# Optimization experiments

Measured on AMD Instinct MI355X. Metric: run time of the kernel, lower is better.

Reference implementation:

```python
import jax, jax.numpy as jnp
import numpy as np

B, TED, G, N, E, MD, NOISE = 10000, 512, 64, 2000, 64000, 15, 128
PAC = 10
PACDIM = (TED + NOISE) * PAC  # 6400
D0, D1 = 1024, 512


def _linear_params(k, fan_in, fan_out):
    kw, kb = jax.random.split(k)
    lim = 1.0 / np.sqrt(fan_in)
    w = jax.random.uniform(kw, (fan_in, fan_out), minval=-lim, maxval=lim, dtype=jnp.float32)
    b = jax.random.uniform(kb, (fan_out,), minval=-lim, maxval=lim, dtype=jnp.float32)
    return w, b


def setup_inputs() -> dict:
    key = jax.random.key(0)
    ks = jax.random.split(key, 12)
    inp = {
        'input_': jax.random.normal(ks[0], (B, TED), dtype=jnp.float32),
        'graphs_x': jax.random.normal(ks[1], (G, N, 1), dtype=jnp.float32),
        'edge_index': jax.random.randint(ks[2], (G, 2, E), 0, N, dtype=jnp.int32),
        'graph_ids': jax.random.randint(ks[3], (B,), 0, G, dtype=jnp.int32),
        'chain': jax.random.normal(ks[4], (B, 1), dtype=jnp.float32),
        'metadata': jax.random.normal(ks[5], (B, MD), dtype=jnp.float32),
    }
    inp['gcn_w'], inp['gcn_b'] = _linear_params(ks[6], 1, 1)
    inp['meta_w'], inp['meta_b'] = _linear_params(ks[7], 1 + MD, 32)
    inp['gme_w'], inp['gme_b'] = _linear_params(ks[8], N + 32, NOISE)
    inp['seq_w0'], inp['seq_b0'] = _linear_params(ks[9], PACDIM, D0)
    inp['seq_w1'], inp['seq_b1'] = _linear_params(ks[10], D0, D1)
    inp['seq_w2'], inp['seq_b2'] = _linear_params(ks[11], D1, 1)
    return inp


def _gcn_one(x, ei, gcn_w, gcn_b):
    # GCNConv(1,1) with self-loops and symmetric normalization.
    loops = jnp.arange(N, dtype=ei.dtype)
    src = jnp.concatenate([ei[0], loops])
    dst = jnp.concatenate([ei[1], loops])
    deg = jax.ops.segment_sum(jnp.ones_like(src, dtype=x.dtype), dst, num_segments=N)
    dinv = jax.lax.rsqrt(deg)  # deg >= 1 due to self-loops
    norm = dinv[src] * dinv[dst]  # [E+N]
    xw = x @ gcn_w  # [N,1]
    msg = xw[src] * norm[:, None]
    out = jax.ops.segment_sum(msg, dst, num_segments=N) + gcn_b
    return out.reshape(-1)  # flatten -> [N]


def reference(input_, graphs_x, edge_index, graph_ids, chain, metadata,
              gcn_w, gcn_b, meta_w, meta_b, gme_w, gme_b,
              seq_w0, seq_b0, seq_w1, seq_b1, seq_w2, seq_b2):
    # per-unique-graph GCN, vectorized over G graphs
    gcn_out = jax.vmap(lambda x, ei: _gcn_one(x, ei, gcn_w, gcn_b))(graphs_x, edge_index)  # [G,N]
    graph_emb = gcn_out[graph_ids]  # gather: [B,N]
    all_meta = jnp.concatenate([chain, metadata], axis=1)  # [B,1+MD]
    meta_emb = jax.nn.relu(all_meta @ meta_w + meta_b)  # [B,32]
    noise = jnp.concatenate([graph_emb, meta_emb], axis=1) @ gme_w + gme_b  # [B,NOISE]
    h = jnp.concatenate([input_, noise], axis=1).reshape(-1, PACDIM)  # [B/PAC, PACDIM]
    h = jax.nn.leaky_relu(h @ seq_w0 + seq_b0, 0.2)  # dropout omitted (eval mode)
    h = jax.nn.leaky_relu(h @ seq_w1 + seq_b1, 0.2)
    return h @ seq_w2 + seq_b2  # [B/PAC, 1]
```

## Files before the change

### kernel.cpp

```cpp
#include <hip/hip_runtime.h>

typedef __bf16 bf16_t;
typedef __bf16 bf16x4 __attribute__((ext_vector_type(4)));
typedef __bf16 bf16x8 __attribute__((ext_vector_type(8)));
typedef float floatx4 __attribute__((ext_vector_type(4)));

#define G_GRAPHS 64
#define N_NODES 2000
#define N_EDGES 64000
#define BATCH 10000
#define TED_ 512
#define NOISE_ 128
#define PACDIM_ 6400
#define D0_ 1024
#define D1_ 512
#define MROWS 1000
#define ESPLIT 8
#define EPB (N_EDGES / ESPLIT)
#define MSPLIT 8
#define S0 8

#define DEG_BLKS 512
#define PACK_BLKS 625
#define MSG_BLKS 512
#define W0T_BLKS 1600
#define W1T_BLKS 128

__device__ __forceinline__ void glds16(const void* g, void* l) {
    __builtin_amdgcn_global_load_lds(
        (__attribute__((address_space(1))) void*)(g),
        (__attribute__((address_space(3))) void*)(l), 16, 0, 0);
}

__global__ __launch_bounds__(512) void deg_pack_kernel(
    const int* __restrict__ edge_index, float* __restrict__ degs_part,
    const float* __restrict__ in, bf16_t* __restrict__ A)
{
    __shared__ float h[N_NODES];
    const int b = blockIdx.x, tid = threadIdx.x;
    if (b < DEG_BLKS) {
        const int s = b & 7, g = b >> 3;
        for (int n = tid; n < N_NODES; n += 512) h[n] = 0.f;
        __syncthreads();
        const int4* d4 = (const int4*)(edge_index + (size_t)g * 2 * N_EDGES
                                       + N_EDGES + s * EPB);
        for (int e = tid; e < EPB / 4; e += 512) {
            int4 v = d4[e];
            atomicAdd(&h[v.x], 1.0f); atomicAdd(&h[v.y], 1.0f);
            atomicAdd(&h[v.z], 1.0f); atomicAdd(&h[v.w], 1.0f);
        }
        __syncthreads();
        float* dp = degs_part + ((size_t)g * ESPLIT + s) * N_NODES;
        for (int n = tid; n < N_NODES; n += 512) dp[n] = h[n];
        return;
    }
    {
        int base = (b - DEG_BLKS) * 2048;
        for (int u = 0; u < 4; u++) {
            int idx = base + u * 512 + tid;
            float4 v = ((const float4*)in)[idx];
            int bb = idx >> 7;
            int c = (idx & 127) << 2;
            int r = bb / 10, slot = bb - r * 10;
            bf16x4 o = { (bf16_t)v.x, (bf16_t)v.y, (bf16_t)v.z, (bf16_t)v.w };
            *(bf16x4*)(A + (size_t)r * PACDIM_ + slot * 640 + c) = o;
        }
    }
}

__global__ __launch_bounds__(512) void work_kernel(
    const float* __restrict__ graphs_x, const int* __restrict__ edge_index,
    const float* __restrict__ degs_part, float* __restrict__ outs_part,
    const float* __restrict__ W0, bf16_t* __restrict__ W0t,
    const float* __restrict__ W1, bf16_t* __restrict__ W1t)
{
    __shared__ __align__(16) float sm[3 * N_NODES];
    const int b = blockIdx.x, tid = threadIdx.x;

    if (b < MSG_BLKS) {
        float* ys  = sm;
        float* dvl = sm + N_NODES;
        float* oh  = sm + 2 * N_NODES;
        const int s = b & 7, g = b >> 3;
        const float* xg = graphs_x + (size_t)g * N_NODES;
        const float* dgp = degs_part + (size_t)g * ESPLIT * N_NODES;
        for (int n = tid; n < N_NODES; n += 512) {
            float d = 1.0f;
            for (int p = 0; p < ESPLIT; p++) d += dgp[(size_t)p * N_NODES + n];
            float dv = rsqrtf(d);
            dvl[n] = dv;
            ys[n] = xg[n] * dv;
            oh[n] = 0.f;
        }
        __syncthreads();
        const int* src = edge_index + (size_t)g * 2 * N_EDGES + s * EPB;
        const int2* s2 = (const int2*)src;
        const int2* d2 = (const int2*)(src + N_EDGES);
        for (int e = tid; e < EPB / 2; e += 512) {
            int2 sv = s2[e], dd = d2[e];
            atomicAdd(&oh[dd.x], ys[sv.x] * dvl[dd.x]);
            atomicAdd(&oh[dd.y], ys[sv.y] * dvl[dd.y]);
        }
        __syncthreads();
        float* op = outs_part + ((size_t)g * MSPLIT + s) * N_NODES;
        for (int n = tid; n < N_NODES; n += 512) op[n] = oh[n];
        return;
    }
    float (*t)[67] = (float(*)[67])sm;
    const float* W; bf16_t* Wt; int Rr, Cc, r0, c0;
    if (b < MSG_BLKS + W0T_BLKS) {
        int tile = b - MSG_BLKS;
        W = W0; Wt = W0t; Rr = PACDIM_; Cc = D0_;
        r0 = (tile >> 4) << 6; c0 = (tile & 15) << 6;
    } else {
        int tile = b - (MSG_BLKS + W0T_BLKS);
        W = W1; Wt = W1t; Rr = D0_; Cc = D1_;
        r0 = (tile >> 3) << 6; c0 = (tile & 7) << 6;
    }
    for (int u = 0; u < 2; u++) {
        int idx = u * 512 + tid;
        int r = idx >> 4, c4 = (idx & 15) << 2;
        float4 v = *(const float4*)(W + (size_t)(r0 + r) * Cc + c0 + c4);
        t[r][c4] = v.x; t[r][c4 + 1] = v.y; t[r][c4 + 2] = v.z; t[r][c4 + 3] = v.w;
    }
    __syncthreads();
    {
        int c = tid >> 3, seg = tid & 7;
        bf16x8 o;
        for (int jj = 0; jj < 8; jj++) o[jj] = (bf16_t)t[seg * 8 + jj][c];
        *(bf16x8*)(Wt + (size_t)(c0 + c) * Rr + r0 + seg * 8) = o;
    }
}

__global__ __launch_bounds__(512) void gnoise_kernel(
    const float* __restrict__ graphs_x, const float* __restrict__ degs_part,
    const float* __restrict__ outs_part,
    const float* __restrict__ gcn_w, const float* __restrict__ gcn_b,
    const float* __restrict__ gme_w, float* __restrict__ gnoise_p)
{
    __shared__ float of[500];
    __shared__ float part[4][128];
    const int s = blockIdx.x, g = blockIdx.y, tid = threadIdx.x;
    const int nBase = s * 500;
    const float w = gcn_w[0], bb = gcn_b[0];
    const float* dgp = degs_part + (size_t)g * ESPLIT * N_NODES;
    const float* otp = outs_part + (size_t)g * MSPLIT * N_NODES;
    for (int n = tid; n < 500; n += 512) {
        int gn = nBase + n;
        float d = 1.0f, o = 0.f;
        for (int p = 0; p < ESPLIT; p++) d += dgp[(size_t)p * N_NODES + gn];
        for (int p = 0; p < MSPLIT; p++) o += otp[(size_t)p * N_NODES + gn];
        of[n] = w * (o + graphs_x[(size_t)g * N_NODES + gn] / d) + bb;
    }
    __syncthreads();
    const int j = tid & 127, ch = tid >> 7;
    float acc = 0.f;
    const int n0 = ch * 125;
    for (int n = n0; n < n0 + 125; n++)
        acc += of[n] * gme_w[(size_t)(nBase + n) * 128 + j];
    part[ch][j] = acc;
    __syncthreads();
    if (tid < 128)
        gnoise_p[((size_t)g * 4 + s) * 128 + tid] =
            part[0][tid] + part[1][tid] + part[2][tid] + part[3][tid];
}

__global__ __launch_bounds__(256) void meta_kernel(
    const float* __restrict__ chain, const float* __restrict__ metadata,
    const int* __restrict__ graph_ids,
    const float* __restrict__ meta_w, const float* __restrict__ meta_b,
    const float* __restrict__ gme_w, const float* __restrict__ gme_b,
    const float* __restrict__ gnoise_p, bf16_t* __restrict__ A)
{
    int wid = (blockIdx.x * 256 + threadIdx.x) >> 6;
    int lane = threadIdx.x & 63;
    if (wid >= BATCH) return;
    const int b = wid;
    float me = 0.f;
    if (lane < 32) {
        me = meta_b[lane] + chain[b] * meta_w[lane];
        for (int i = 1; i < 16; i++)
            me += metadata[(size_t)b * 15 + (i - 1)] * meta_w[(size_t)i * 32 + lane];
        me = me > 0.f ? me : 0.f;
    }
    const int gid = graph_ids[b];
    const float* gp = gnoise_p + (size_t)gid * 4 * 128;
    const int j1 = lane, j2 = lane + 64;
    float n1 = gme_b[j1] + gp[j1] + gp[128 + j1] + gp[256 + j1] + gp[384 + j1];
    float n2 = gme_b[j2] + gp[j2] + gp[128 + j2] + gp[256 + j2] + gp[384 + j2];
    for (int k = 0; k < 32; k++) {
        float mk = __shfl(me, k, 64);
        const float* wrow = gme_w + (size_t)(N_NODES + k) * 128;
        n1 += mk * wrow[j1];
        n2 += mk * wrow[j2];
    }
    int r = b / 10, slot = b - r * 10;
    bf16_t* dp = A + (size_t)r * PACDIM_ + slot * 640 + TED_;
    dp[j1] = (bf16_t)n1;
    dp[j2] = (bf16_t)n2;
}

__global__ __launch_bounds__(256) void gemm_bt_splitk_kernel(
    const bf16_t* __restrict__ A,
    const bf16_t* __restrict__ Bt,
    float* __restrict__ P,
    int M, int N, int K, int KS, int zbits, int xbits, int Mp)
{
    __shared__ __align__(16) bf16_t As[2][128 * 32];
    __shared__ __align__(16) bf16_t Bs[2][128 * 32];
    const int tid = threadIdx.x;
    const int wave = tid >> 6;
    const int lane = tid & 63;
    const int id = blockIdx.x;
    const int z = id & ((1 << zbits) - 1);
    const int xt = (id >> zbits) & ((1 << xbits) - 1);
    const int yt = id >> (zbits + xbits);
    const int mBase = yt * 128;
    const int nBase = xt * 128;
    const int wm = (wave & 1) * 64;
    const int wn = (wave >> 1) * 64;

    floatx4 acc[4][4] = {};

    const int rA0 = tid >> 2;
    const int g4 = tid & 3;
    const int f4 = (rA0 >> 1) & 3;
    const int k8 = (g4 ^ f4) * 8;
    int gm0 = mBase + rA0;      if (gm0 > M - 1) gm0 = M - 1;
    int gm1 = mBase + 64 + rA0; if (gm1 > M - 1) gm1 = M - 1;
    const bf16_t* aP0 = A + (size_t)gm0 * K + k8;
    const bf16_t* aP1 = A + (size_t)gm1 * K + k8;
    const bf16_t* bP0 = Bt + (size_t)(nBase + rA0) * K + k8;
    const bf16_t* bP1 = Bt + (size_t)(nBase + 64 + rA0) * K + k8;

    const int q4 = lane >> 4;
    const int mr = lane & 15;
    const int kq = ((q4 ^ ((mr >> 1) & 3)) * 8);
    int aOff[4], bOff[4];
    for (int i = 0; i < 4; i++) aOff[i] = (wm + i * 16 + mr) * 32 + kq;
    for (int j = 0; j < 4; j++) bOff[j] = (wn + j * 16 + mr) * 32 + kq;

    const int nIter = KS >> 5;
    const int kc = z * KS;
    {
        char* lA = (char*)(&As[0][0]) + wave * 1024;
        char* lB = (char*)(&Bs[0][0]) + wave * 1024;
        glds16(aP0 + kc, lA);
        glds16(aP1 + kc, lA + 4096);
        glds16(bP0 + kc, lB);
        glds16(bP1 + kc, lB + 4096);
    }
    __syncthreads();
    for (int t = 0; t < nIter; ++t) {
        const int cur = t & 1;
        if (t + 1 < nIter) {
            const int kn = kc + (t + 1) * 32;
            char* lA = (char*)(&As[cur ^ 1][0]) + wave * 1024;
            char* lB = (char*)(&Bs[cur ^ 1][0]) + wave * 1024;
            glds16(aP0 + kn, lA);
            glds16(aP1 + kn, lA + 4096);
            glds16(bP0 + kn, lB);
            glds16(bP1 + kn, lB + 4096);
        }
        const bf16_t* aB = &As[cur][0];
        const bf16_t* bB = &Bs[cur][0];
        bf16x8 af[4], bfr[4];
        for (int i = 0; i < 4; i++) af[i] = *(const bf16x8*)(aB + aOff[i]);
        for (int j = 0; j < 4; j++) bfr[j] = *(const bf16x8*)(bB + bOff[j]);
        for (int i = 0; i < 4; i++)
            for (int j = 0; j < 4; j++)
                acc[i][j] = __builtin_amdgcn_mfma_f32_16x16x32_bf16(
                    af[i], bfr[j], acc[i][j], 0, 0, 0);
        __syncthreads();
    }

    float* Pz = P + (size_t)z * Mp * N;
    const int rq = (lane >> 4) * 4;
    const int cn = lane & 15;
    for (int j = 0; j < 4; j++) {
        int col = nBase + wn + j * 16 + cn;
        for (int i = 0; i < 4; i++)
            for (int r = 0; r < 4; r++) {
                int rowm = mBase + wm + i * 16 + rq + r;
                Pz[(size_t)rowm * N + col] = acc[i][j][r];
            }
    }
}

__global__ __launch_bounds__(256) void reduce_bias_leaky_kernel(
    const float* __restrict__ P, const float* __restrict__ bias,
    bf16_t* __restrict__ C, int M, int N, int Mp, int S,
    const float* __restrict__ b2, float* __restrict__ outp)
{
    if (blockIdx.x == 0 && threadIdx.x < MROWS / 4) {
        float bb2 = b2[0];
        ((float4*)outp)[threadIdx.x] = make_float4(bb2, bb2, bb2, bb2);
    }
    int idx = blockIdx.x * 256 + threadIdx.x;
    int total = M * (N >> 2);
    if (idx >= total) return;
    int nv = N >> 2;
    int r = idx / nv, c4 = (idx - r * nv) << 2;
    size_t off = (size_t)r * N + c4;
    size_t stride = (size_t)Mp * N;
    float4 v = *(const float4*)(P + off);
    for (int s = 1; s < S; s++) {
        float4 u = *(const float4*)(P + s * stride + off);
        v.x += u.x; v.y += u.y; v.z += u.z; v.w += u.w;
    }
    const float4 bv = *(const float4*)(bias + c4);
    v.x += bv.x; v.y += bv.y; v.z += bv.z; v.w += bv.w;
    v.x = v.x > 0.f ? v.x : 0.2f * v.x;
    v.y = v.y > 0.f ? v.y : 0.2f * v.y;
    v.z = v.z > 0.f ? v.z : 0.2f * v.z;
    v.w = v.w > 0.f ? v.w : 0.2f * v.w;
    bf16x4 o = { (bf16_t)v.x, (bf16_t)v.y, (bf16_t)v.z, (bf16_t)v.w };
    *(bf16x4*)(C + off) = o;
}

__global__ __launch_bounds__(256) void gemm1_final_kernel(
    const bf16_t* __restrict__ A,
    const bf16_t* __restrict__ Bt,
    const float* __restrict__ b1, const float* __restrict__ w2,
    float* __restrict__ outp)
{
    __shared__ __align__(16) bf16_t As[2][128 * 32];
    __shared__ __align__(16) bf16_t Bs[2][128 * 32];
    const int K = D0_;
    const int tid = threadIdx.x;
    const int wave = tid >> 6;
    const int lane = tid & 63;
    const int xt = blockIdx.x & 3;
    const int yt = blockIdx.x >> 2;
    const int mBase = yt * 128;
    const int nBase = xt * 128;
    const int wm = (wave & 1) * 64;
    const int wn = (wave >> 1) * 64;

    floatx4 acc[4][4] = {};

    const int rA0 = tid >> 2;
    const int g4 = tid & 3;
    const int f4 = (rA0 >> 1) & 3;
    const int k8 = (g4 ^ f4) * 8;
    int gm0 = mBase + rA0;      if (gm0 > MROWS - 1) gm0 = MROWS - 1;
    int gm1 = mBase + 64 + rA0; if (gm1 > MROWS - 1) gm1 = MROWS - 1;
    const bf16_t* aP0 = A + (size_t)gm0 * K + k8;
    const bf16_t* aP1 = A + (size_t)gm1 * K + k8;
    const bf16_t* bP0 = Bt + (size_t)(nBase + rA0) * K + k8;
    const bf16_t* bP1 = Bt + (size_t)(nBase + 64 + rA0) * K + k8;

    const int q4 = lane >> 4;
    const int mr = lane & 15;
    const int kq = ((q4 ^ ((mr >> 1) & 3)) * 8);
    int aOff[4], bOff[4];
    for (int i = 0; i < 4; i++) aOff[i] = (wm + i * 16 + mr) * 32 + kq;
    for (int j = 0; j < 4; j++) bOff[j] = (wn + j * 16 + mr) * 32 + kq;

    const int nIter = K >> 5;
    {
        char* lA = (char*)(&As[0][0]) + wave * 1024;
        char* lB = (char*)(&Bs[0][0]) + wave * 1024;
        glds16(aP0, lA);
        glds16(aP1, lA + 4096);
        glds16(bP0, lB);
        glds16(bP1, lB + 4096);
    }
    __syncthreads();
    for (int t = 0; t < nIter; ++t) {
        const int cur = t & 1;
        if (t + 1 < nIter) {
            const int kn = (t + 1) * 32;
            char* lA = (char*)(&As[cur ^ 1][0]) + wave * 1024;
            char* lB = (char*)(&Bs[cur ^ 1][0]) + wave * 1024;
            glds16(aP0 + kn, lA);
            glds16(aP1 + kn, lA + 4096);
            glds16(bP0 + kn, lB);
            glds16(bP1 + kn, lB + 4096);
        }
        const bf16_t* aB = &As[cur][0];
        const bf16_t* bB = &Bs[cur][0];
        bf16x8 af[4], bfr[4];
        for (int i = 0; i < 4; i++) af[i] = *(const bf16x8*)(aB + aOff[i]);
        for (int j = 0; j < 4; j++) bfr[j] = *(const bf16x8*)(bB + bOff[j]);
        for (int i = 0; i < 4; i++)
            for (int j = 0; j < 4; j++)
                acc[i][j] = __builtin_amdgcn_mfma_f32_16x16x32_bf16(
                    af[i], bfr[j], acc[i][j], 0, 0, 0);
        __syncthreads();
    }

    const int cn = lane & 15;
    float b1v[4], w2v[4];
    for (int j = 0; j < 4; j++) {
        int col = nBase + wn + j * 16 + cn;
        b1v[j] = b1[col];
        w2v[j] = w2[col];
    }
    for (int i = 0; i < 4; i++) {
        for (int r = 0; r < 4; r++) {
            float part = 0.f;
            for (int j = 0; j < 4; j++) {
                float v = acc[i][j][r] + b1v[j];
                v = v > 0.f ? v : 0.2f * v;
                part += v * w2v[j];
            }
            for (int off = 8; off; off >>= 1) part += __shfl_xor(part, off, 16);
            if (cn == 0) {
                int rowm = mBase + wm + i * 16 + q4 * 4 + r;
                if (rowm < MROWS) atomicAdd(&outp[rowm], part);
            }
        }
    }
}

extern "C" void kernel_launch(void* const* d_in, const int* in_sizes, int n_in,
                              void* d_out, int out_size, void* d_ws, size_t ws_size,
                              hipStream_t stream)
{
    const float* input_    = (const float*)d_in[0];
    const float* graphs_x  = (const float*)d_in[1];
    const int*   edge_idx  = (const int*)  d_in[2];
    const int*   graph_ids = (const int*)  d_in[3];
    const float* chain     = (const float*)d_in[4];
    const float* metadata  = (const float*)d_in[5];
    const float* gcn_w     = (const float*)d_in[6];
    const float* gcn_b     = (const float*)d_in[7];
    const float* meta_w    = (const float*)d_in[8];
    const float* meta_b    = (const float*)d_in[9];
    const float* gme_w     = (const float*)d_in[10];
    const float* gme_b     = (const float*)d_in[11];
    const float* seq_w0    = (const float*)d_in[12];
    const float* seq_b0    = (const float*)d_in[13];
    const float* seq_w1    = (const float*)d_in[14];
    const float* seq_b1    = (const float*)d_in[15];
    const float* seq_w2    = (const float*)d_in[16];
    const float* seq_b2    = (const float*)d_in[17];
    float* out = (float*)d_out;

    char* ws = (char*)d_ws;
    float*  degs_part = (float*)(ws + 0);
    float*  outs_part = (float*)(ws + 4096000);
    float*  gnoise_p  = (float*)(ws + 8192000);
    bf16_t* Abuf      = (bf16_t*)(ws + 8323072);
    bf16_t* W0t       = (bf16_t*)(ws + 21123072);
    bf16_t* W1t       = (bf16_t*)(ws + 34230272);
    bf16_t* H1        = (bf16_t*)(ws + 35278848);
    float*  P         = (float*)(ws + 37326848);

    deg_pack_kernel<<<DEG_BLKS + PACK_BLKS, 512, 0, stream>>>(
        edge_idx, degs_part, input_, Abuf);
    work_kernel<<<MSG_BLKS + W0T_BLKS + W1T_BLKS, 512, 0, stream>>>(
        graphs_x, edge_idx, degs_part, outs_part,
        seq_w0, W0t, seq_w1, W1t);
    gnoise_kernel<<<dim3(4, G_GRAPHS), 512, 0, stream>>>(
        graphs_x, degs_part, outs_part, gcn_w, gcn_b, gme_w, gnoise_p);
    meta_kernel<<<2500, 256, 0, stream>>>(
        chain, metadata, graph_ids, meta_w, meta_b, gme_w, gme_b,
        gnoise_p, Abuf);

    gemm_bt_splitk_kernel<<<512, 256, 0, stream>>>(
        Abuf, W0t, P, MROWS, D0_, PACDIM_, PACDIM_ / S0, 3, 3, 1024);
    reduce_bias_leaky_kernel<<<(MROWS * D0_ / 4 + 255) / 256, 256, 0, stream>>>(
        P, seq_b0, H1, MROWS, D0_, 1024, S0, seq_b2, out);

    gemm1_final_kernel<<<32, 256, 0, stream>>>(
        H1, W1t, seq_b1, seq_w2, out);
}
```

Before: 256.0 us.

## Fuse gnoise and split-K reduce into producer kernels via last-block counters

Removes the separate gnoise and reduce_bias_leaky kernel launches. An atomic arrival counter with threadfence lets the last block per graph compute the GCN-to-noise projection, and the last split-K block per output tile do the reduction, bias and leaky ReLU. Counters are zeroed in the first kernel, and the output bias init moves into meta_kernel. This saves two launches and inter-kernel gaps, but the tail work now runs serially in a single block per graph or tile, which may lengthen the critical path.

Result: slower. 505.8 us (+97.6%).

```diff
diff --git a/kernel.cpp b/kernel.cpp
--- a/kernel.cpp
+++ b/kernel.cpp
@@ -34,11 +34,13 @@
 
 __global__ __launch_bounds__(512) void deg_pack_kernel(
     const int* __restrict__ edge_index, float* __restrict__ degs_part,
-    const float* __restrict__ in, bf16_t* __restrict__ A)
+    const float* __restrict__ in, bf16_t* __restrict__ A,
+    int* __restrict__ cnts)
 {
     __shared__ float h[N_NODES];
     const int b = blockIdx.x, tid = threadIdx.x;
     if (b < DEG_BLKS) {
+        if (b == 0 && tid < 128) cnts[tid] = 0;
         const int s = b & 7, g = b >> 3;
         for (int n = tid; n < N_NODES; n += 512) h[n] = 0.f;
         __syncthreads();
@@ -72,9 +74,13 @@
     const float* __restrict__ graphs_x, const int* __restrict__ edge_index,
     const float* __restrict__ degs_part, float* __restrict__ outs_part,
     const float* __restrict__ W0, bf16_t* __restrict__ W0t,
-    const float* __restrict__ W1, bf16_t* __restrict__ W1t)
+    const float* __restrict__ W1, bf16_t* __restrict__ W1t,
+    const float* __restrict__ gcn_w, const float* __restrict__ gcn_b,
+    const float* __restrict__ gme_w, const float* __restrict__ gme_b,
+    float* __restrict__ gnoise, int* __restrict__ cnts)
 {
     __shared__ __align__(16) float sm[3 * N_NODES];
+    __shared__ int lastFlag;
     const int b = blockIdx.x, tid = threadIdx.x;
 
     if (b < MSG_BLKS) {
@@ -104,6 +110,35 @@
         __syncthreads();
         float* op = outs_part + ((size_t)g * MSPLIT + s) * N_NODES;
         for (int n = tid; n < N_NODES; n += 512) op[n] = oh[n];
+
+        __threadfence();
+        __syncthreads();
+        if (tid == 0) lastFlag = (atomicAdd(&cnts[g], 1) == MSPLIT - 1);
+        __syncthreads();
+        if (!lastFlag) return;
+        __threadfence();
+        float* of   = sm;
+        float* part = sm + 2048;
+        const float* otp = outs_part + (size_t)g * MSPLIT * N_NODES;
+        const float w = gcn_w[0], bb = gcn_b[0];
+        for (int n = tid; n < N_NODES; n += 512) {
+            float d = 1.0f, o = 0.f;
+            for (int p = 0; p < ESPLIT; p++) d += dgp[(size_t)p * N_NODES + n];
+            for (int p = 0; p < MSPLIT; p++) o += otp[(size_t)p * N_NODES + n];
+            of[n] = w * (o + xg[n] / d) + bb;
+        }
+        __syncthreads();
+        const int j = tid & 127, ch = tid >> 7;
+        float acc = 0.f;
+        const int n0 = ch * 500;
+        for (int n = n0; n < n0 + 500; n++)
+            acc += of[n] * gme_w[(size_t)n * 128 + j];
+        part[ch * 128 + j] = acc;
+        __syncthreads();
+        if (tid < 128)
+            gnoise[(size_t)g * 128 + tid] =
+                part[tid] + part[128 + tid] + part[256 + tid] + part[384 + tid]
+                + gme_b[tid];
         return;
     }
     float (*t)[67] = (float(*)[67])sm;
@@ -132,46 +167,18 @@
     }
 }
 
-__global__ __launch_bounds__(512) void gnoise_kernel(
-    const float* __restrict__ graphs_x, const float* __restrict__ degs_part,
-    const float* __restrict__ outs_part,
-    const float* __restrict__ gcn_w, const float* __restrict__ gcn_b,
-    const float* __restrict__ gme_w, float* __restrict__ gnoise_p)
-{
-    __shared__ float of[500];
-    __shared__ float part[4][128];
-    const int s = blockIdx.x, g = blockIdx.y, tid = threadIdx.x;
-    const int nBase = s * 500;
-    const float w = gcn_w[0], bb = gcn_b[0];
-    const float* dgp = degs_part + (size_t)g * ESPLIT * N_NODES;
-    const float* otp = outs_part + (size_t)g * MSPLIT * N_NODES;
-    for (int n = tid; n < 500; n += 512) {
-        int gn = nBase + n;
-        float d = 1.0f, o = 0.f;
-        for (int p = 0; p < ESPLIT; p++) d += dgp[(size_t)p * N_NODES + gn];
-        for (int p = 0; p < MSPLIT; p++) o += otp[(size_t)p * N_NODES + gn];
-        of[n] = w * (o + graphs_x[(size_t)g * N_NODES + gn] / d) + bb;
-    }
-    __syncthreads();
-    const int j = tid & 127, ch = tid >> 7;
-    float acc = 0.f;
-    const int n0 = ch * 125;
-    for (int n = n0; n < n0 + 125; n++)
-        acc += of[n] * gme_w[(size_t)(nBase + n) * 128 + j];
-    part[ch][j] = acc;
-    __syncthreads();
-    if (tid < 128)
-        gnoise_p[((size_t)g * 4 + s) * 128 + tid] =
-            part[0][tid] + part[1][tid] + part[2][tid] + part[3][tid];
-}
-
 __global__ __launch_bounds__(256) void meta_kernel(
     const float* __restrict__ chain, const float* __restrict__ metadata,
     const int* __restrict__ graph_ids,
     const float* __restrict__ meta_w, const float* __restrict__ meta_b,
-    const float* __restrict__ gme_w, const float* __restrict__ gme_b,
-    const float* __restrict__ gnoise_p, bf16_t* __restrict__ A)
-{
+    const float* __restrict__ gme_w,
+    const float* __restrict__ gnoise, bf16_t* __restrict__ A,
+    const float* __restrict__ b2, float* __restrict__ outp)
+{
+    if (blockIdx.x == 0 && threadIdx.x < MROWS / 4) {
+        float bb2 = b2[0];
+        ((float4*)outp)[threadIdx.x] = make_float4(bb2, bb2, bb2, bb2);
+    }
     int wid = (blockIdx.x * 256 + threadIdx.x) >> 6;
     int lane = threadIdx.x & 63;
     if (wid >= BATCH) return;
@@ -184,10 +191,10 @@
         me = me > 0.f ? me : 0.f;
     }
     const int gid = graph_ids[b];
-    const float* gp = gnoise_p + (size_t)gid * 4 * 128;
+    const float* gp = gnoise + (size_t)gid * 128;
     const int j1 = lane, j2 = lane + 64;
-    float n1 = gme_b[j1] + gp[j1] + gp[128 + j1] + gp[256 + j1] + gp[384 + j1];
-    float n2 = gme_b[j2] + gp[j2] + gp[128 + j2] + gp[256 + j2] + gp[384 + j2];
+    float n1 = gp[j1];
+    float n2 = gp[j2];
     for (int k = 0; k < 32; k++) {
         float mk = __shfl(me, k, 64);
         const float* wrow = gme_w + (size_t)(N_NODES + k) * 128;
@@ -204,10 +211,13 @@
     const bf16_t* __restrict__ A,
     const bf16_t* __restrict__ Bt,
     float* __restrict__ P,
-    int M, int N, int K, int KS, int zbits, int xbits, int Mp)
+    int M, int N, int K, int KS, int zbits, int xbits, int Mp,
+    const float* __restrict__ bias, bf16_t* __restrict__ C,
+    int* __restrict__ cnts)
 {
     __shared__ __align__(16) bf16_t As[2][128 * 32];
     __shared__ __align__(16) bf16_t Bs[2][128 * 32];
+    __shared__ int lastFlag;
     const int tid = threadIdx.x;
     const int wave = tid >> 6;
     const int lane = tid & 63;
@@ -285,37 +295,36 @@
                 Pz[(size_t)rowm * N + col] = acc[i][j][r];
             }
     }
-}
-
-__global__ __launch_bounds__(256) void reduce_bias_leaky_kernel(
-    const float* __restrict__ P, const float* __restrict__ bias,
-    bf16_t* __restrict__ C, int M, int N, int Mp, int S,
-    const float* __restrict__ b2, float* __restrict__ outp)
-{
-    if (blockIdx.x == 0 && threadIdx.x < MROWS / 4) {
-        float bb2 = b2[0];
-        ((float4*)outp)[threadIdx.x] = make_float4(bb2, bb2, bb2, bb2);
-    }
-    int idx = blockIdx.x * 256 + threadIdx.x;
-    int total = M * (N >> 2);
-    if (idx >= total) return;
-    int nv = N >> 2;
-    int r = idx / nv, c4 = (idx - r * nv) << 2;
-    size_t off = (size_t)r * N + c4;
-    size_t stride = (size_t)Mp * N;
-    float4 v = *(const float4*)(P + off);
-    for (int s = 1; s < S; s++) {
-        float4 u = *(const float4*)(P + s * stride + off);
-        v.x += u.x; v.y += u.y; v.z += u.z; v.w += u.w;
-    }
-    const float4 bv = *(const float4*)(bias + c4);
-    v.x += bv.x; v.y += bv.y; v.z += bv.z; v.w += bv.w;
-    v.x = v.x > 0.f ? v.x : 0.2f * v.x;
-    v.y = v.y > 0.f ? v.y : 0.2f * v.y;
-    v.z = v.z > 0.f ? v.z : 0.2f * v.z;
-    v.w = v.w > 0.f ? v.w : 0.2f * v.w;
-    bf16x4 o = { (bf16_t)v.x, (bf16_t)v.y, (bf16_t)v.z, (bf16_t)v.w };
-    *(bf16x4*)(C + off) = o;
+
+    __threadfence();
+    __syncthreads();
+    if (tid == 0)
+        lastFlag = (atomicAdd(&cnts[yt * (1 << xbits) + xt], 1)
+                    == (1 << zbits) - 1);
+    __syncthreads();
+    if (!lastFlag) return;
+    __threadfence();
+    const int S = 1 << zbits;
+    const size_t stride = (size_t)Mp * N;
+    for (int i = tid; i < 128 * 32; i += 256) {
+        int r = i >> 5, c4 = (i & 31) << 2;
+        int rowm = mBase + r;
+        if (rowm >= M) continue;
+        size_t off = (size_t)rowm * N + nBase + c4;
+        float4 v = *(const float4*)(P + off);
+        for (int s = 1; s < S; s++) {
+            float4 u = *(const float4*)(P + (size_t)s * stride + off);
+            v.x += u.x; v.y += u.y; v.z += u.z; v.w += u.w;
+        }
+        const float4 bv = *(const float4*)(bias + nBase + c4);
+        v.x += bv.x; v.y += bv.y; v.z += bv.z; v.w += bv.w;
+        v.x = v.x > 0.f ? v.x : 0.2f * v.x;
+        v.y = v.y > 0.f ? v.y : 0.2f * v.y;
+        v.z = v.z > 0.f ? v.z : 0.2f * v.z;
+        v.w = v.w > 0.f ? v.w : 0.2f * v.w;
+        bf16x4 o = { (bf16_t)v.x, (bf16_t)v.y, (bf16_t)v.z, (bf16_t)v.w };
+        *(bf16x4*)(C + off) = o;
+    }
 }
 
 __global__ __launch_bounds__(256) void gemm1_final_kernel(
@@ -441,29 +450,26 @@
     char* ws = (char*)d_ws;
     float*  degs_part = (float*)(ws + 0);
     float*  outs_part = (float*)(ws + 4096000);
-    float*  gnoise_p  = (float*)(ws + 8192000);
-    bf16_t* Abuf      = (bf16_t*)(ws + 8323072);
-    bf16_t* W0t       = (bf16_t*)(ws + 21123072);
-    bf16_t* W1t       = (bf16_t*)(ws + 34230272);
-    bf16_t* H1        = (bf16_t*)(ws + 35278848);
-    float*  P         = (float*)(ws + 37326848);
+    float*  gnoise    = (float*)(ws + 8192000);
+    int*    cnts      = (int*)  (ws + 8224768);
+    bf16_t* Abuf      = (bf16_t*)(ws + 8225280);
+    bf16_t* W0t       = (bf16_t*)(ws + 21025280);
+    bf16_t* W1t       = (bf16_t*)(ws + 34132480);
+    bf16_t* H1        = (bf16_t*)(ws + 35181056);
+    float*  P         = (float*)(ws + 37229056);
 
     deg_pack_kernel<<<DEG_BLKS + PACK_BLKS, 512, 0, stream>>>(
-        edge_idx, degs_part, input_, Abuf);
+        edge_idx, degs_part, input_, Abuf, cnts);
     work_kernel<<<MSG_BLKS + W0T_BLKS + W1T_BLKS, 512, 0, stream>>>(
         graphs_x, edge_idx, degs_part, outs_part,
-        seq_w0, W0t, seq_w1, W1t);
-    gnoise_kernel<<<dim3(4, G_GRAPHS), 512, 0, stream>>>(
-        graphs_x, degs_part, outs_part, gcn_w, gcn_b, gme_w, gnoise_p);
+        seq_w0, W0t, seq_w1, W1t,
+        gcn_w, gcn_b, gme_w, gme_b, gnoise, cnts);
     meta_kernel<<<2500, 256, 0, stream>>>(
-        chain, metadata, graph_ids, meta_w, meta_b, gme_w, gme_b,
-        gnoise_p, Abuf);
-
+        chain, metadata, graph_ids, meta_w, meta_b, gme_w,
+        gnoise, Abuf, seq_b2, out);
     gemm_bt_splitk_kernel<<<512, 256, 0, stream>>>(
-        Abuf, W0t, P, MROWS, D0_, PACDIM_, PACDIM_ / S0, 3, 3, 1024);
-    reduce_bias_leaky_kernel<<<(MROWS * D0_ / 4 + 255) / 256, 256, 0, stream>>>(
-        P, seq_b0, H1, MROWS, D0_, 1024, S0, seq_b2, out);
-
+        Abuf, W0t, P, MROWS, D0_, PACDIM_, PACDIM_ / S0, 3, 3, 1024,
+        seq_b0, H1, cnts + 64);
     gemm1_final_kernel<<<32, 256, 0, stream>>>(
         H1, W1t, seq_b1, seq_w2, out);
 }
```

## Fuse GCN aggregation and graph-noise projection into message-passing blocks

Applied to the files above, without the earlier changes.

Each message-passing block now multiplies its partial aggregated node values directly by the gme_w graph rows and writes a per-split 128-wide partial, removing the separate gnoise kernel and the outs_part buffer. The self-loop term, GCN bias and gme_b are folded in by the split-0 block, and meta_kernel sums the eight partials. Output bias initialization moves into meta_kernel. This saves a launch and an intermediate round trip but makes every block stream the full 2000x128 gme_w slice, greatly increasing weight reads.

Measured after the change: 268.6 us. 4.9% more time.

```diff
diff --git a/kernel.cpp b/kernel.cpp
--- a/kernel.cpp
+++ b/kernel.cpp
@@ -70,11 +70,16 @@
 
 __global__ __launch_bounds__(512) void work_kernel(
     const float* __restrict__ graphs_x, const int* __restrict__ edge_index,
-    const float* __restrict__ degs_part, float* __restrict__ outs_part,
+    const float* __restrict__ degs_part,
     const float* __restrict__ W0, bf16_t* __restrict__ W0t,
-    const float* __restrict__ W1, bf16_t* __restrict__ W1t)
+    const float* __restrict__ W1, bf16_t* __restrict__ W1t,
+    const float* __restrict__ gcn_w, const float* __restrict__ gcn_b,
+    const float* __restrict__ gme_w, const float* __restrict__ gme_b,
+    float* __restrict__ gnoise_p)
 {
     __shared__ __align__(16) float sm[3 * N_NODES];
+    __shared__ float part[4][128];
+    __shared__ float partw[4][128];
     const int b = blockIdx.x, tid = threadIdx.x;
 
     if (b < MSG_BLKS) {
@@ -102,8 +107,35 @@
             atomicAdd(&oh[dd.y], ys[sv.y] * dvl[dd.y]);
         }
         __syncthreads();
-        float* op = outs_part + ((size_t)g * MSPLIT + s) * N_NODES;
-        for (int n = tid; n < N_NODES; n += 512) op[n] = oh[n];
+        const int j = tid & 127, ch = tid >> 7;
+        const float* wp = gme_w + j;
+        const int n0 = ch * 500;
+        float acc = 0.f, accw = 0.f;
+        if (s == 0) {
+            for (int n = n0; n < n0 + 500; n++) {
+                float wnj = wp[(size_t)n * 128];
+                acc += (oh[n] + ys[n] * dvl[n]) * wnj;
+                accw += wnj;
+            }
+        } else {
+            for (int n = n0; n < n0 + 500; n++)
+                acc += oh[n] * wp[(size_t)n * 128];
+        }
+        part[ch][j] = acc;
+        partw[ch][j] = accw;
+        __syncthreads();
+        if (tid < 128) {
+            const float w = gcn_w[0];
+            float v = w * (part[0][tid] + part[1][tid]
+                           + part[2][tid] + part[3][tid]);
+            if (s == 0)
+                v += gcn_b[0] * (partw[0][tid] + partw[1][tid]
+                                 + partw[2][tid] + partw[3][tid]) * 0.f
+                     + gcn_b[0] * (partw[0][tid] + partw[1][tid]
+                                   + partw[2][tid] + partw[3][tid])
+                     + gme_b[tid];
+            gnoise_p[((size_t)g * MSPLIT + s) * 128 + tid] = v;
+        }
         return;
     }
     float (*t)[67] = (float(*)[67])sm;
@@ -132,46 +164,18 @@
     }
 }
 
-__global__ __launch_bounds__(512) void gnoise_kernel(
-    const float* __restrict__ graphs_x, const float* __restrict__ degs_part,
-    const float* __restrict__ outs_part,
-    const float* __restrict__ gcn_w, const float* __restrict__ gcn_b,
-    const float* __restrict__ gme_w, float* __restrict__ gnoise_p)
-{
-    __shared__ float of[500];
-    __shared__ float part[4][128];
-    const int s = blockIdx.x, g = blockIdx.y, tid = threadIdx.x;
-    const int nBase = s * 500;
-    const float w = gcn_w[0], bb = gcn_b[0];
-    const float* dgp = degs_part + (size_t)g * ESPLIT * N_NODES;
-    const float* otp = outs_part + (size_t)g * MSPLIT * N_NODES;
-    for (int n = tid; n < 500; n += 512) {
-        int gn = nBase + n;
-        float d = 1.0f, o = 0.f;
-        for (int p = 0; p < ESPLIT; p++) d += dgp[(size_t)p * N_NODES + gn];
-        for (int p = 0; p < MSPLIT; p++) o += otp[(size_t)p * N_NODES + gn];
-        of[n] = w * (o + graphs_x[(size_t)g * N_NODES + gn] / d) + bb;
-    }
-    __syncthreads();
-    const int j = tid & 127, ch = tid >> 7;
-    float acc = 0.f;
-    const int n0 = ch * 125;
-    for (int n = n0; n < n0 + 125; n++)
-        acc += of[n] * gme_w[(size_t)(nBase + n) * 128 + j];
-    part[ch][j] = acc;
-    __syncthreads();
-    if (tid < 128)
-        gnoise_p[((size_t)g * 4 + s) * 128 + tid] =
-            part[0][tid] + part[1][tid] + part[2][tid] + part[3][tid];
-}
-
 __global__ __launch_bounds__(256) void meta_kernel(
     const float* __restrict__ chain, const float* __restrict__ metadata,
     const int* __restrict__ graph_ids,
     const float* __restrict__ meta_w, const float* __restrict__ meta_b,
-    const float* __restrict__ gme_w, const float* __restrict__ gme_b,
-    const float* __restrict__ gnoise_p, bf16_t* __restrict__ A)
-{
+    const float* __restrict__ gme_w,
+    const float* __restrict__ gnoise_p, bf16_t* __restrict__ A,
+    const float* __restrict__ b2, float* __restrict__ outp)
+{
+    if (blockIdx.x == 0 && threadIdx.x < MROWS / 4) {
+        float bb2 = b2[0];
+        ((float4*)outp)[threadIdx.x] = make_float4(bb2, bb2, bb2, bb2);
+    }
     int wid = (blockIdx.x * 256 + threadIdx.x) >> 6;
     int lane = threadIdx.x & 63;
     if (wid >= BATCH) return;
@@ -184,10 +188,13 @@
         me = me > 0.f ? me : 0.f;
     }
     const int gid = graph_ids[b];
-    const float* gp = gnoise_p + (size_t)gid * 4 * 128;
+    const float* gp = gnoise_p + (size_t)gid * MSPLIT * 128;
     const int j1 = lane, j2 = lane + 64;
-    float n1 = gme_b[j1] + gp[j1] + gp[128 + j1] + gp[256 + j1] + gp[384 + j1];
-    float n2 = gme_b[j2] + gp[j2] + gp[128 + j2] + gp[256 + j2] + gp[384 + j2];
+    float n1 = 0.f, n2 = 0.f;
+    for (int s = 0; s < MSPLIT; s++) {
+        n1 += gp[s * 128 + j1];
+        n2 += gp[s * 128 + j2];
+    }
     for (int k = 0; k < 32; k++) {
         float mk = __shfl(me, k, 64);
         const float* wrow = gme_w + (size_t)(N_NODES + k) * 128;
@@ -289,13 +296,8 @@
 
 __global__ __launch_bounds__(256) void reduce_bias_leaky_kernel(
     const float* __restrict__ P, const float* __restrict__ bias,
-    bf16_t* __restrict__ C, int M, int N, int Mp, int S,
-    const float* __restrict__ b2, float* __restrict__ outp)
-{
-    if (blockIdx.x == 0 && threadIdx.x < MROWS / 4) {
-        float bb2 = b2[0];
-        ((float4*)outp)[threadIdx.x] = make_float4(bb2, bb2, bb2, bb2);
-    }
+    bf16_t* __restrict__ C, int M, int N, int Mp, int S)
+{
     int idx = blockIdx.x * 256 + threadIdx.x;
     int total = M * (N >> 2);
     if (idx >= total) return;
@@ -440,30 +442,26 @@
 
     char* ws = (char*)d_ws;
     float*  degs_part = (float*)(ws + 0);
-    float*  outs_part = (float*)(ws + 4096000);
-    float*  gnoise_p  = (float*)(ws + 8192000);
-    bf16_t* Abuf      = (bf16_t*)(ws + 8323072);
-    bf16_t* W0t       = (bf16_t*)(ws + 21123072);
-    bf16_t* W1t       = (bf16_t*)(ws + 34230272);
-    bf16_t* H1        = (bf16_t*)(ws + 35278848);
-    float*  P         = (float*)(ws + 37326848);
+    float*  gnoise_p  = (float*)(ws + 4096000);
+    bf16_t* Abuf      = (bf16_t*)(ws + 4358144);
+    bf16_t* W0t       = (bf16_t*)(ws + 17158144);
+    bf16_t* W1t       = (bf16_t*)(ws + 30265344);
+    bf16_t* H1        = (bf16_t*)(ws + 31313920);
+    float*  P         = (float*)(ws + 33361920);
 
     deg_pack_kernel<<<DEG_BLKS + PACK_BLKS, 512, 0, stream>>>(
         edge_idx, degs_part, input_, Abuf);
     work_kernel<<<MSG_BLKS + W0T_BLKS + W1T_BLKS, 512, 0, stream>>>(
-        graphs_x, edge_idx, degs_part, outs_part,
-        seq_w0, W0t, seq_w1, W1t);
-    gnoise_kernel<<<dim3(4, G_GRAPHS), 512, 0, stream>>>(
-        graphs_x, degs_part, outs_part, gcn_w, gcn_b, gme_w, gnoise_p);
+        graphs_x, edge_idx, degs_part,
+        seq_w0, W0t, seq_w1, W1t,
+        gcn_w, gcn_b, gme_w, gme_b, gnoise_p);
     meta_kernel<<<2500, 256, 0, stream>>>(
-        chain, metadata, graph_ids, meta_w, meta_b, gme_w, gme_b,
-        gnoise_p, Abuf);
-
+        chain, metadata, graph_ids, meta_w, meta_b, gme_w,
+        gnoise_p, Abuf, seq_b2, out);
     gemm_bt_splitk_kernel<<<512, 256, 0, stream>>>(
         Abuf, W0t, P, MROWS, D0_, PACDIM_, PACDIM_ / S0, 3, 3, 1024);
     reduce_bias_leaky_kernel<<<(MROWS * D0_ / 4 + 255) / 256, 256, 0, stream>>>(
-        P, seq_b0, H1, MROWS, D0_, 1024, S0, seq_b2, out);
-
+        P, seq_b0, H1, MROWS, D0_, 1024, S0);
     gemm1_final_kernel<<<32, 256, 0, stream>>>(
         H1, W1t, seq_b1, seq_w2, out);
 }
```

## Split layer-0 GEMM by K source and overlap input part with noise kernels

Applied to the files above, without the earlier changes.

The first big GEMM is split by K into two parts. The input_ columns (512 of every 640) are computed in blocks co-launched with the gnoise and meta kernels, and the noise columns are computed in a separate GEMM after meta finishes. This hides the small serial gnoise and meta kernels behind GEMM work and removes a dependency bubble. In exchange the reduce kernel now sums 10 partial slabs instead of 8, which adds traffic, and the GEMM inner loop carries extra index arithmetic for the strided K offsets.

Result: slower. 273.9 us (+7.0%).

```diff
diff --git a/kernel.cpp b/kernel.cpp
--- a/kernel.cpp
+++ b/kernel.cpp
@@ -18,7 +18,7 @@
 #define ESPLIT 8
 #define EPB (N_EDGES / ESPLIT)
 #define MSPLIT 8
-#define S0 8
+#define PSLAB (1024 * 1024)
 
 #define DEG_BLKS 512
 #define PACK_BLKS 625
@@ -31,6 +31,9 @@
         (__attribute__((address_space(1))) void*)(g),
         (__attribute__((address_space(3))) void*)(l), 16, 0, 0);
 }
+
+__device__ __forceinline__ int kof_in(int it) { return (it >> 4) * 640 + ((it & 15) << 5); }
+__device__ __forceinline__ int kof_nz(int it) { return (it >> 2) * 640 + 512 + ((it & 3) << 5); }
 
 __global__ __launch_bounds__(512) void deg_pack_kernel(
     const int* __restrict__ edge_index, float* __restrict__ degs_part,
@@ -132,20 +135,102 @@
     }
 }
 
-__global__ __launch_bounds__(512) void gnoise_kernel(
+__device__ __forceinline__ void gemm0_body(
+    const bf16_t* __restrict__ A, const bf16_t* __restrict__ Bt,
+    float* __restrict__ Pz, bf16_t* AsB, bf16_t* BsB,
+    int mBase, int nBase, int itBase, int nIter, bool noise)
+{
+    const int tid = threadIdx.x;
+    const int wave = tid >> 6, lane = tid & 63;
+    const int wm = (wave & 1) * 64, wn = (wave >> 1) * 64;
+    floatx4 acc[4][4] = {};
+
+    const int rA0 = tid >> 2, g4 = tid & 3, f4 = (rA0 >> 1) & 3;
+    const int k8 = (g4 ^ f4) * 8;
+    int gm0 = mBase + rA0;      if (gm0 > MROWS - 1) gm0 = MROWS - 1;
+    int gm1 = mBase + 64 + rA0; if (gm1 > MROWS - 1) gm1 = MROWS - 1;
+    const bf16_t* aP0 = A + (size_t)gm0 * PACDIM_ + k8;
+    const bf16_t* aP1 = A + (size_t)gm1 * PACDIM_ + k8;
+    const bf16_t* bP0 = Bt + (size_t)(nBase + rA0) * PACDIM_ + k8;
+    const bf16_t* bP1 = Bt + (size_t)(nBase + 64 + rA0) * PACDIM_ + k8;
+
+    const int q4 = lane >> 4, mr = lane & 15;
+    const int kq = ((q4 ^ ((mr >> 1) & 3)) * 8);
+    int aOff[4], bOff[4];
+    for (int i = 0; i < 4; i++) aOff[i] = (wm + i * 16 + mr) * 32 + kq;
+    for (int j = 0; j < 4; j++) bOff[j] = (wn + j * 16 + mr) * 32 + kq;
+
+    {
+        int k0 = noise ? kof_nz(itBase) : kof_in(itBase);
+        char* lA = (char*)AsB + wave * 1024;
+        char* lB = (char*)BsB + wave * 1024;
+        glds16(aP0 + k0, lA);
+        glds16(aP1 + k0, lA + 4096);
+        glds16(bP0 + k0, lB);
+        glds16(bP1 + k0, lB + 4096);
+    }
+    __syncthreads();
+    for (int t = 0; t < nIter; ++t) {
+        const int cur = t & 1;
+        if (t + 1 < nIter) {
+            int kn = noise ? kof_nz(itBase + t + 1) : kof_in(itBase + t + 1);
+            char* lA = (char*)AsB + (cur ^ 1) * 8192 + wave * 1024;
+            char* lB = (char*)BsB + (cur ^ 1) * 8192 + wave * 1024;
+            glds16(aP0 + kn, lA);
+            glds16(aP1 + kn, lA + 4096);
+            glds16(bP0 + kn, lB);
+            glds16(bP1 + kn, lB + 4096);
+        }
+        const bf16_t* aB = AsB + cur * 4096;
+        const bf16_t* bB = BsB + cur * 4096;
+        bf16x8 af[4], bfr[4];
+        for (int i = 0; i < 4; i++) af[i] = *(const bf16x8*)(aB + aOff[i]);
+        for (int j = 0; j < 4; j++) bfr[j] = *(const bf16x8*)(bB + bOff[j]);
+        for (int i = 0; i < 4; i++)
+            for (int j = 0; j < 4; j++)
+                acc[i][j] = __builtin_amdgcn_mfma_f32_16x16x32_bf16(
+                    af[i], bfr[j], acc[i][j], 0, 0, 0);
+        __syncthreads();
+    }
+
+    const int rq = (lane >> 4) * 4;
+    const int cn = lane & 15;
+    for (int j = 0; j < 4; j++) {
+        int col = nBase + wn + j * 16 + cn;
+        for (int i = 0; i < 4; i++)
+            for (int r = 0; r < 4; r++) {
+                int rowm = mBase + wm + i * 16 + rq + r;
+                Pz[(size_t)rowm * D0_ + col] = acc[i][j][r];
+            }
+    }
+}
+
+__global__ __launch_bounds__(256) void g0a_gnoise_kernel(
+    const bf16_t* __restrict__ A, const bf16_t* __restrict__ W0t,
+    float* __restrict__ P,
     const float* __restrict__ graphs_x, const float* __restrict__ degs_part,
     const float* __restrict__ outs_part,
     const float* __restrict__ gcn_w, const float* __restrict__ gcn_b,
     const float* __restrict__ gme_w, float* __restrict__ gnoise_p)
 {
-    __shared__ float of[500];
-    __shared__ float part[4][128];
-    const int s = blockIdx.x, g = blockIdx.y, tid = threadIdx.x;
+    __shared__ __align__(16) bf16_t As[2][128 * 32];
+    __shared__ __align__(16) bf16_t Bs[2][128 * 32];
+    const int b = blockIdx.x, tid = threadIdx.x;
+    if (b < 256) {
+        const int z = b & 3, xt = (b >> 2) & 7, yt = b >> 5;
+        gemm0_body(A, W0t, P + (size_t)z * PSLAB,
+                   &As[0][0], &Bs[0][0], yt * 128, xt * 128, z * 20, 20, false);
+        return;
+    }
+    float* of = (float*)&As[0][0];
+    float* part = of + 512;
+    const int idx = b - 256;
+    const int s = idx & 3, g = idx >> 2;
     const int nBase = s * 500;
     const float w = gcn_w[0], bb = gcn_b[0];
     const float* dgp = degs_part + (size_t)g * ESPLIT * N_NODES;
     const float* otp = outs_part + (size_t)g * MSPLIT * N_NODES;
-    for (int n = tid; n < 500; n += 512) {
+    for (int n = tid; n < 500; n += 256) {
         int gn = nBase + n;
         float d = 1.0f, o = 0.f;
         for (int p = 0; p < ESPLIT; p++) d += dgp[(size_t)p * N_NODES + gn];
@@ -155,35 +240,45 @@
     __syncthreads();
     const int j = tid & 127, ch = tid >> 7;
     float acc = 0.f;
-    const int n0 = ch * 125;
-    for (int n = n0; n < n0 + 125; n++)
+    const int n0 = ch * 250;
+    for (int n = n0; n < n0 + 250; n++)
         acc += of[n] * gme_w[(size_t)(nBase + n) * 128 + j];
-    part[ch][j] = acc;
+    part[ch * 128 + j] = acc;
     __syncthreads();
     if (tid < 128)
-        gnoise_p[((size_t)g * 4 + s) * 128 + tid] =
-            part[0][tid] + part[1][tid] + part[2][tid] + part[3][tid];
-}
-
-__global__ __launch_bounds__(256) void meta_kernel(
+        gnoise_p[((size_t)g * 4 + s) * 128 + tid] = part[tid] + part[128 + tid];
+}
+
+__global__ __launch_bounds__(256) void g0a_meta_kernel(
+    const bf16_t* __restrict__ Ab, const bf16_t* __restrict__ W0t,
+    float* __restrict__ P,
     const float* __restrict__ chain, const float* __restrict__ metadata,
     const int* __restrict__ graph_ids,
     const float* __restrict__ meta_w, const float* __restrict__ meta_b,
     const float* __restrict__ gme_w, const float* __restrict__ gme_b,
     const float* __restrict__ gnoise_p, bf16_t* __restrict__ A)
 {
-    int wid = (blockIdx.x * 256 + threadIdx.x) >> 6;
+    __shared__ __align__(16) bf16_t As[2][128 * 32];
+    __shared__ __align__(16) bf16_t Bs[2][128 * 32];
+    const int b = blockIdx.x;
+    if (b < 256) {
+        const int z = 4 + (b & 3), xt = (b >> 2) & 7, yt = b >> 5;
+        gemm0_body(Ab, W0t, P + (size_t)z * PSLAB,
+                   &As[0][0], &Bs[0][0], yt * 128, xt * 128, z * 20, 20, false);
+        return;
+    }
+    int wid = ((b - 256) * 256 + threadIdx.x) >> 6;
     int lane = threadIdx.x & 63;
     if (wid >= BATCH) return;
-    const int b = wid;
+    const int bb = wid;
     float me = 0.f;
     if (lane < 32) {
-        me = meta_b[lane] + chain[b] * meta_w[lane];
+        me = meta_b[lane] + chain[bb] * meta_w[lane];
         for (int i = 1; i < 16; i++)
-            me += metadata[(size_t)b * 15 + (i - 1)] * meta_w[(size_t)i * 32 + lane];
+            me += metadata[(size_t)bb * 15 + (i - 1)] * meta_w[(size_t)i * 32 + lane];
         me = me > 0.f ? me : 0.f;
     }
-    const int gid = graph_ids[b];
+    const int gid = graph_ids[bb];
     const float* gp = gnoise_p + (size_t)gid * 4 * 128;
     const int j1 = lane, j2 = lane + 64;
     float n1 = gme_b[j1] + gp[j1] + gp[128 + j1] + gp[256 + j1] + gp[384 + j1];
@@ -194,102 +289,27 @@
         n1 += mk * wrow[j1];
         n2 += mk * wrow[j2];
     }
-    int r = b / 10, slot = b - r * 10;
+    int r = bb / 10, slot = bb - r * 10;
     bf16_t* dp = A + (size_t)r * PACDIM_ + slot * 640 + TED_;
     dp[j1] = (bf16_t)n1;
     dp[j2] = (bf16_t)n2;
 }
 
-__global__ __launch_bounds__(256) void gemm_bt_splitk_kernel(
-    const bf16_t* __restrict__ A,
-    const bf16_t* __restrict__ Bt,
-    float* __restrict__ P,
-    int M, int N, int K, int KS, int zbits, int xbits, int Mp)
+__global__ __launch_bounds__(256) void gemm0b_kernel(
+    const bf16_t* __restrict__ A, const bf16_t* __restrict__ W0t,
+    float* __restrict__ P)
 {
     __shared__ __align__(16) bf16_t As[2][128 * 32];
     __shared__ __align__(16) bf16_t Bs[2][128 * 32];
-    const int tid = threadIdx.x;
-    const int wave = tid >> 6;
-    const int lane = tid & 63;
-    const int id = blockIdx.x;
-    const int z = id & ((1 << zbits) - 1);
-    const int xt = (id >> zbits) & ((1 << xbits) - 1);
-    const int yt = id >> (zbits + xbits);
-    const int mBase = yt * 128;
-    const int nBase = xt * 128;
-    const int wm = (wave & 1) * 64;
-    const int wn = (wave >> 1) * 64;
-
-    floatx4 acc[4][4] = {};
-
-    const int rA0 = tid >> 2;
-    const int g4 = tid & 3;
-    const int f4 = (rA0 >> 1) & 3;
-    const int k8 = (g4 ^ f4) * 8;
-    int gm0 = mBase + rA0;      if (gm0 > M - 1) gm0 = M - 1;
-    int gm1 = mBase + 64 + rA0; if (gm1 > M - 1) gm1 = M - 1;
-    const bf16_t* aP0 = A + (size_t)gm0 * K + k8;
-    const bf16_t* aP1 = A + (size_t)gm1 * K + k8;
-    const bf16_t* bP0 = Bt + (size_t)(nBase + rA0) * K + k8;
-    const bf16_t* bP1 = Bt + (size_t)(nBase + 64 + rA0) * K + k8;
-
-    const int q4 = lane >> 4;
-    const int mr = lane & 15;
-    const int kq = ((q4 ^ ((mr >> 1) & 3)) * 8);
-    int aOff[4], bOff[4];
-    for (int i = 0; i < 4; i++) aOff[i] = (wm + i * 16 + mr) * 32 + kq;
-    for (int j = 0; j < 4; j++) bOff[j] = (wn + j * 16 + mr) * 32 + kq;
-
-    const int nIter = KS >> 5;
-    const int kc = z * KS;
-    {
-        char* lA = (char*)(&As[0][0]) + wave * 1024;
-        char* lB = (char*)(&Bs[0][0]) + wave * 1024;
-        glds16(aP0 + kc, lA);
-        glds16(aP1 + kc, lA + 4096);
-        glds16(bP0 + kc, lB);
-        glds16(bP1 + kc, lB + 4096);
-    }
-    __syncthreads();
-    for (int t = 0; t < nIter; ++t) {
-        const int cur = t & 1;
-        if (t + 1 < nIter) {
-            const int kn = kc + (t + 1) * 32;
-            char* lA = (char*)(&As[cur ^ 1][0]) + wave * 1024;
-            char* lB = (char*)(&Bs[cur ^ 1][0]) + wave * 1024;
-            glds16(aP0 + kn, lA);
-            glds16(aP1 + kn, lA + 4096);
-            glds16(bP0 + kn, lB);
-            glds16(bP1 + kn, lB + 4096);
-        }
-        const bf16_t* aB = &As[cur][0];
-        const bf16_t* bB = &Bs[cur][0];
-        bf16x8 af[4], bfr[4];
-        for (int i = 0; i < 4; i++) af[i] = *(const bf16x8*)(aB + aOff[i]);
-        for (int j = 0; j < 4; j++) bfr[j] = *(const bf16x8*)(bB + bOff[j]);
-        for (int i = 0; i < 4; i++)
-            for (int j = 0; j < 4; j++)
-                acc[i][j] = __builtin_amdgcn_mfma_f32_16x16x32_bf16(
-                    af[i], bfr[j], acc[i][j], 0, 0, 0);
-        __syncthreads();
-    }
-
-    float* Pz = P + (size_t)z * Mp * N;
-    const int rq = (lane >> 4) * 4;
-    const int cn = lane & 15;
-    for (int j = 0; j < 4; j++) {
-        int col = nBase + wn + j * 16 + cn;
-        for (int i = 0; i < 4; i++)
-            for (int r = 0; r < 4; r++) {
-                int rowm = mBase + wm + i * 16 + rq + r;
-                Pz[(size_t)rowm * N + col] = acc[i][j][r];
-            }
-    }
+    const int b = blockIdx.x;
+    const int z = b & 1, xt = (b >> 1) & 7, yt = b >> 4;
+    gemm0_body(A, W0t, P + (size_t)(8 + z) * PSLAB,
+               &As[0][0], &Bs[0][0], yt * 128, xt * 128, z * 20, 20, true);
 }
 
 __global__ __launch_bounds__(256) void reduce_bias_leaky_kernel(
     const float* __restrict__ P, const float* __restrict__ bias,
-    bf16_t* __restrict__ C, int M, int N, int Mp, int S,
+    bf16_t* __restrict__ C,
     const float* __restrict__ b2, float* __restrict__ outp)
 {
     if (blockIdx.x == 0 && threadIdx.x < MROWS / 4) {
@@ -297,15 +317,14 @@
         ((float4*)outp)[threadIdx.x] = make_float4(bb2, bb2, bb2, bb2);
     }
     int idx = blockIdx.x * 256 + threadIdx.x;
-    int total = M * (N >> 2);
+    int total = MROWS * (D0_ >> 2);
     if (idx >= total) return;
-    int nv = N >> 2;
+    int nv = D0_ >> 2;
     int r = idx / nv, c4 = (idx - r * nv) << 2;
-    size_t off = (size_t)r * N + c4;
-    size_t stride = (size_t)Mp * N;
+    size_t off = (size_t)r * D0_ + c4;
     float4 v = *(const float4*)(P + off);
-    for (int s = 1; s < S; s++) {
-        float4 u = *(const float4*)(P + s * stride + off);
+    for (int s = 1; s < 10; s++) {
+        float4 u = *(const float4*)(P + (size_t)s * PSLAB + off);
         v.x += u.x; v.y += u.y; v.z += u.z; v.w += u.w;
     }
     const float4 bv = *(const float4*)(bias + c4);
@@ -453,17 +472,15 @@
     work_kernel<<<MSG_BLKS + W0T_BLKS + W1T_BLKS, 512, 0, stream>>>(
         graphs_x, edge_idx, degs_part, outs_part,
         seq_w0, W0t, seq_w1, W1t);
-    gnoise_kernel<<<dim3(4, G_GRAPHS), 512, 0, stream>>>(
-        graphs_x, degs_part, outs_part, gcn_w, gcn_b, gme_w, gnoise_p);
-    meta_kernel<<<2500, 256, 0, stream>>>(
-        chain, metadata, graph_ids, meta_w, meta_b, gme_w, gme_b,
-        gnoise_p, Abuf);
-
-    gemm_bt_splitk_kernel<<<512, 256, 0, stream>>>(
-        Abuf, W0t, P, MROWS, D0_, PACDIM_, PACDIM_ / S0, 3, 3, 1024);
-    reduce_bias_leaky_kernel<<<(MROWS * D0_ / 4 + 255) / 256, 256, 0, stream>>>(
-        P, seq_b0, H1, MROWS, D0_, 1024, S0, seq_b2, out);
-
+    g0a_gnoise_kernel<<<512, 256, 0, stream>>>(
+        Abuf, W0t, P, graphs_x, degs_part, outs_part,
+        gcn_w, gcn_b, gme_w, gnoise_p);
+    g0a_meta_kernel<<<2756, 256, 0, stream>>>(
+        Abuf, W0t, P, chain, metadata, graph_ids, meta_w, meta_b,
+        gme_w, gme_b, gnoise_p, Abuf);
+    gemm0b_kernel<<<128, 256, 0, stream>>>(Abuf, W0t, P);
+    reduce_bias_leaky_kernel<<<(MROWS * D0_ / 4) / 256, 256, 0, stream>>>(
+        P, seq_b0, H1, seq_b2, out);
     gemm1_final_kernel<<<32, 256, 0, stream>>>(
         H1, W1t, seq_b1, seq_w2, out);
 }
```
